# Kernel tuning notes

Hardware: AMD Instinct MI355X
Metric: run time of the kernel (lower is better)

The kernel has to match this reference:

```python
import jax, jax.numpy as jnp
import numpy as np
from jax import lax

N, D, H, O = 16384, 512, 1024, 512
G, E, K = 3, 4, 2
ALPHA = 0.01


def setup_inputs() -> dict:
    key = jax.random.key(0)
    ks = jax.random.split(key, 16)

    def lin(k, out_d, in_d):
        s = 1.0 / np.sqrt(in_d)
        return jax.random.uniform(k, (out_d, in_d), jnp.float32, -s, s)

    x = jax.random.normal(ks[0], (N, D), jnp.float32)
    Wm = lin(ks[1], G, D)
    bm = jnp.zeros((G,), jnp.float32)
    # group routers stacked: [G, E, D]
    Wr = jax.random.uniform(ks[2], (G, E, D), jnp.float32, -1 / np.sqrt(D), 1 / np.sqrt(D))
    br = jnp.zeros((G, E), jnp.float32)
    # expert params stacked over (group, expert)
    W1 = jax.random.uniform(ks[3], (G, E, H, D), jnp.float32, -1 / np.sqrt(D), 1 / np.sqrt(D))
    b1 = jnp.zeros((G, E, H), jnp.float32)
    W2 = jax.random.uniform(ks[4], (G, E, H, H), jnp.float32, -1 / np.sqrt(H), 1 / np.sqrt(H))
    b2 = jnp.zeros((G, E, H), jnp.float32)
    Wp = jax.random.uniform(ks[5], (G, E, H, D), jnp.float32, -1 / np.sqrt(D), 1 / np.sqrt(D))
    bp = jnp.zeros((G, E, H), jnp.float32)
    W3 = jax.random.uniform(ks[6], (G, E, O, H), jnp.float32, -1 / np.sqrt(H), 1 / np.sqrt(H))
    b3 = jnp.zeros((G, E, O), jnp.float32)
    return {"x": x, "Wm": Wm, "bm": bm, "Wr": Wr, "br": br,
            "W1": W1, "b1": b1, "W2": W2, "b2": b2,
            "Wp": Wp, "bp": bp, "W3": W3, "b3": b3}


def _expert(x, W1, b1, W2, b2, Wp, bp, W3, b3):
    # residual MLP (dropout in eval mode => identity)
    h = jax.nn.relu(x @ W1.T + b1)
    h = h @ W2.T + b2
    ident = x @ Wp.T + bp  # projection (input_dim != hidden_dim)
    h = jax.nn.relu(h + ident)
    return h @ W3.T + b3


def reference(x, Wm, bm, Wr, br, W1, b1, W2, b2, Wp, bp, W3, b3):
    n = x.shape[0]
    # ---- meta (top-1 group) routing ----
    meta_logits = x @ Wm.T + bm                         # [N, G]
    g = jnp.argmax(meta_logits, axis=1)                 # top-1 group per token
    pm = jax.nn.softmax(meta_logits, axis=1).mean(0)    # [G]
    aux = ALPHA * G * jnp.sum(pm * pm)
    # ---- per-group router logits, gathered for each token's group ----
    logits_all = jnp.einsum('nd,ged->nge', x, Wr) + br  # [N, G, E]
    sel = jnp.take_along_axis(logits_all, g[:, None, None], axis=1)[:, 0, :]  # [N, E]
    # ---- group-level load-balancing aux loss (over tokens in each group) ----
    probs = jax.nn.softmax(sel, axis=-1)                # [N, E]
    onehot_g = (g[:, None] == jnp.arange(G)[None, :])   # [N, G] bool
    cnt = onehot_g.sum(0)                               # [G]
    mean_g = (onehot_g.astype(x.dtype).T @ probs) / jnp.maximum(cnt, 1)[:, None].astype(x.dtype)
    aux = aux + jnp.sum(jnp.where(cnt > 0, ALPHA * E * jnp.sum(mean_g * mean_g, -1), 0.0))
    # ---- top-k expert weights within selected group (softmax over the k logits) ----
    vals, idx = lax.top_k(sel, K)                       # [N, K]
    w = jax.nn.softmax(vals, axis=-1)                   # [N, K]
    cw = jnp.zeros((n, E), x.dtype).at[jnp.arange(n)[:, None], idx].set(w)   # [N, E]
    combine = cw[:, None, :] * onehot_g[:, :, None].astype(x.dtype)          # [N, G, E]
    # ---- expert compute + combine (loop over the fixed small set of experts) ----
    out = jnp.zeros((n, O), x.dtype)
    for gi in range(G):
        for e in range(E):
            y = _expert(x, W1[gi, e], b1[gi, e], W2[gi, e], b2[gi, e],
                        Wp[gi, e], bp[gi, e], W3[gi, e], b3[gi, e])
            out = out + combine[:, gi, e:e + 1] * y
    return out, aux
```

## Files before the change

kernel.cpp:

```cpp
#include <hip/hip_runtime.h>
#include <hip/hip_bf16.h>

#define N_TOK 16384
#define DDIM  512
#define HDIM  1024
#define ODIM  512
#define NG    3
#define NE    4
#define NGE   12

typedef __bf16 bf16x8 __attribute__((ext_vector_type(8)));
typedef float  f32x4  __attribute__((ext_vector_type(4)));
typedef unsigned int u32;

__device__ __forceinline__ void gld_lds16(const void* gsrc, void* ldst) {
    __builtin_amdgcn_global_load_lds(
        (const __attribute__((address_space(1))) u32*)gsrc,
        (__attribute__((address_space(3))) u32*)ldst, 16, 0, 0);
}

static constexpr size_t OFF_WSLOT = 512;
static constexpr size_t OFF_ELIST = OFF_WSLOT + (size_t)N_TOK*2*4;
static constexpr size_t OFF_XBF   = 1048576;
static constexpr size_t OFF_W1    = OFF_XBF + (size_t)N_TOK*DDIM*2;
static constexpr size_t OFF_W2    = OFF_W1  + (size_t)NGE*HDIM*DDIM*2;
static constexpr size_t OFF_WP    = OFF_W2  + (size_t)NGE*HDIM*HDIM*2;
static constexpr size_t OFF_W3    = OFF_WP  + (size_t)NGE*HDIM*DDIM*2;
static constexpr size_t OFF_H1    = OFF_W3  + (size_t)NGE*ODIM*HDIM*2;
static constexpr size_t OFF_U     = OFF_H1  + (size_t)N_TOK*2*HDIM*2;
static constexpr size_t OFF_Y     = OFF_U   + (size_t)N_TOK*2*HDIM*2;
static constexpr size_t WS_NEED   = OFF_Y   + (size_t)N_TOK*2*ODIM*2;

__global__ void cast_all_k(const float* __restrict__ x,  const float* __restrict__ w1,
                           const float* __restrict__ w2, const float* __restrict__ wp,
                           const float* __restrict__ w3,
                           __bf16* xbf, __bf16* w1b, __bf16* w2b, __bf16* wpb, __bf16* w3b) {
    int tid = blockIdx.x * blockDim.x + threadIdx.x;
    int stride = gridDim.x * blockDim.x;
    auto seg = [&](const float* __restrict__ s, __bf16* __restrict__ d, int n4) {
        const float4* s4 = (const float4*)s;
        uint2* d4 = (uint2*)d;
        for (int i = tid; i < n4; i += stride) {
            float4 v = s4[i];
            union { __bf16 h[4]; uint2 u; } o;
            o.h[0] = (__bf16)v.x; o.h[1] = (__bf16)v.y;
            o.h[2] = (__bf16)v.z; o.h[3] = (__bf16)v.w;
            d4[i] = o.u;
        }
    };
    seg(x,  xbf, N_TOK*DDIM/4);
    seg(w1, w1b, NGE*HDIM*DDIM/4);
    seg(w2, w2b, NGE*HDIM*HDIM/4);
    seg(wp, wpb, NGE*HDIM*DDIM/4);
    seg(w3, w3b, NGE*ODIM*HDIM/4);
}

__global__ __launch_bounds__(256) void routing_k(
        const float* __restrict__ x,  const float* __restrict__ Wm,
        const float* __restrict__ bm, const float* __restrict__ Wr,
        const float* __restrict__ br,
        float* pmsum, float* psum, int* cnt, int* ecount,
        int* elist, float* wslot) {
    __shared__ float lpm[NG];
    __shared__ float lpsum[NGE];
    __shared__ int   lcnt[NG];
    __shared__ int   lec[NGE];
    __shared__ int   lbase[NGE];
    __shared__ int   lentry[NGE][64];

    int tid = threadIdx.x;
    if (tid < NG)  { lpm[tid] = 0.f; lcnt[tid] = 0; }
    if (tid < NGE) { lpsum[tid] = 0.f; lec[tid] = 0; }
    __syncthreads();

    int wid = tid >> 6, lane = tid & 63;

    #pragma unroll 1
    for (int i = 0; i < 16; ++i) {
        int t = blockIdx.x * 64 + i * 4 + wid;

        const float4* xr = (const float4*)(x + (size_t)t * DDIM);
        float4 xa = xr[lane*2], xb = xr[lane*2+1];

        float meta[NG];
        #pragma unroll
        for (int gi = 0; gi < NG; ++gi) {
            const float4* w = (const float4*)(Wm + gi*DDIM);
            float4 wa = w[lane*2], wb = w[lane*2+1];
            float s = xa.x*wa.x + xa.y*wa.y + xa.z*wa.z + xa.w*wa.w
                    + xb.x*wb.x + xb.y*wb.y + xb.z*wb.z + xb.w*wb.w;
            #pragma unroll
            for (int off = 32; off > 0; off >>= 1) s += __shfl_xor(s, off);
            meta[gi] = s + bm[gi];
        }
        int g = 0;
        if (meta[1] > meta[g]) g = 1;
        if (meta[2] > meta[g]) g = 2;

        float mm = fmaxf(meta[0], fmaxf(meta[1], meta[2]));
        float e0 = expf(meta[0]-mm), e1 = expf(meta[1]-mm), e2 = expf(meta[2]-mm);
        float inv = 1.f / (e0 + e1 + e2);

        float sel[NE];
        #pragma unroll
        for (int e = 0; e < NE; ++e) {
            const float4* w = (const float4*)(Wr + (size_t)(g*NE + e)*DDIM);
            float4 wa = w[lane*2], wb = w[lane*2+1];
            float s = xa.x*wa.x + xa.y*wa.y + xa.z*wa.z + xa.w*wa.w
                    + xb.x*wb.x + xb.y*wb.y + xb.z*wb.z + xb.w*wb.w;
            #pragma unroll
            for (int off = 32; off > 0; off >>= 1) s += __shfl_xor(s, off);
            sel[e] = s + br[g*NE + e];
        }
        float ms = fmaxf(fmaxf(sel[0],sel[1]), fmaxf(sel[2],sel[3]));
        float pe[NE]; float ss = 0.f;
        #pragma unroll
        for (int e = 0; e < NE; ++e) { pe[e] = expf(sel[e]-ms); ss += pe[e]; }
        float invs = 1.f / ss;

        int i0 = 0;
        #pragma unroll
        for (int e = 1; e < NE; ++e) if (sel[e] > sel[i0]) i0 = e;
        int i1 = (i0 == 0) ? 1 : 0;
        #pragma unroll
        for (int e = 0; e < NE; ++e) if (e != i0 && sel[e] > sel[i1]) i1 = e;
        float ew = expf(sel[i1] - sel[i0]);
        float wden = 1.f / (1.f + ew);

        if (lane == 0) {
            atomicAdd(&lpm[0], e0*inv);
            atomicAdd(&lpm[1], e1*inv);
            atomicAdd(&lpm[2], e2*inv);
            #pragma unroll
            for (int e = 0; e < NE; ++e) atomicAdd(&lpsum[g*NE + e], pe[e]*invs);
            atomicAdd(&lcnt[g], 1);
            int ee0 = g*NE + i0, ee1 = g*NE + i1;
            int p0 = atomicAdd(&lec[ee0], 1);
            lentry[ee0][p0] = t*2;
            int p1 = atomicAdd(&lec[ee1], 1);
            lentry[ee1][p1] = t*2 + 1;
            wslot[t*2]   = wden;
            wslot[t*2+1] = ew * wden;
        }
    }
    __syncthreads();

    if (tid < NG)  { atomicAdd(pmsum + tid, lpm[tid]); atomicAdd(cnt + tid, lcnt[tid]); }
    if (tid < NGE) { atomicAdd(psum + tid, lpsum[tid]);
                     lbase[tid] = atomicAdd(ecount + tid, lec[tid]); }
    __syncthreads();

    for (int e = wid; e < NGE; e += 4) {
        int c = lec[e], base = lbase[e];
        for (int j = lane; j < c; j += 64)
            elist[e*N_TOK + base + j] = lentry[e][j];
    }
}

__global__ void finalize_aux_k(const float* pmsum, const float* psum, const int* cnt,
                               float* outAux) {
    if (threadIdx.x != 0 || blockIdx.x != 0) return;
    float s = 0.f;
    for (int i = 0; i < NG; ++i) { float p = pmsum[i] / (float)N_TOK; s += p*p; }
    float aux = 0.01f * NG * s;
    for (int gg = 0; gg < NG; ++gg) {
        int c = cnt[gg];
        if (c > 0) {
            float s2 = 0.f;
            for (int e = 0; e < NE; ++e) { float m = psum[gg*NE+e] / (float)c; s2 += m*m; }
            aux += 0.01f * NE * s2;
        }
    }
    *outAux = aux;
}

template<int NDIM, bool RELU, bool TWOPASS>
__global__ __launch_bounds__(256) void expert_gemm_k(
        const __bf16* __restrict__ A1, int shift1, int k1, const __bf16* __restrict__ B1,
        const __bf16* __restrict__ A2, int shift2, int k2, const __bf16* __restrict__ B2,
        const float* __restrict__ bias1, const float* __restrict__ bias2,
        __bf16* __restrict__ Out,
        const int* __restrict__ ecount, const int* __restrict__ elist) {
    int ge = blockIdx.z;
    int cntE = ecount[ge];
    int m0 = blockIdx.x * 128;
    if (m0 >= cntE) return;
    int n0 = blockIdx.y * 128;

    __shared__ __align__(16) char ldsA[16384];
    __shared__ __align__(16) char ldsB[16384];
    __shared__ int ents[128];

    int tid = threadIdx.x;
    if (tid < 128) {
        int r = m0 + tid;
        if (r >= cntE) r = cntE - 1;
        ents[tid] = elist[ge*N_TOK + r];
    }
    __syncthreads();

    int lane = tid & 63, wv = tid >> 6;
    int wm = wv >> 1, wn = wv & 1;
    int lr = lane & 15, lg = lane >> 4;
    int rl = lane >> 3;
    int csw = (lane & 7) ^ rl;
    int rsw = lr & 7;

    f32x4 acc[4][4] = {};

    #pragma unroll
    for (int pass = 0; pass < (TWOPASS ? 2 : 1); ++pass) {
        const __bf16* A  = pass ? A2 : A1;
        const __bf16* Bm = pass ? B2 : B1;
        int kdim  = pass ? k2 : k1;
        int shift = pass ? shift2 : shift1;
        size_t rowB = (size_t)kdim * 2;
        const char* Bbase = (const char*)(Bm + (size_t)ge * NDIM * kdim) + (size_t)n0 * rowB;

        const char* sA[4]; const char* sB[4];
        #pragma unroll
        for (int j = 0; j < 4; ++j) {
            int r = (wv*4 + j)*8 + rl;
            sA[j] = (const char*)A + (size_t)(ents[r] >> shift) * rowB + (size_t)csw*16;
            sB[j] = Bbase + (size_t)r * rowB + (size_t)csw*16;
        }

        for (int kt = 0; kt < kdim; kt += 64) {
            size_t ko = (size_t)kt * 2;
            #pragma unroll
            for (int j = 0; j < 4; ++j) {
                gld_lds16(sA[j] + ko, ldsA + (wv*4 + j)*1024);
                gld_lds16(sB[j] + ko, ldsB + (wv*4 + j)*1024);
            }
            __syncthreads();
            #pragma unroll
            for (int kk = 0; kk < 2; ++kk) {
                bf16x8 av[4], bv[4];
                #pragma unroll
                for (int mi = 0; mi < 4; ++mi) {
                    int ar = wm*64 + mi*16 + lr;
                    av[mi] = *(const bf16x8*)(ldsA + ar*128 + ((((kk*4+lg) ^ rsw)) << 4));
                }
                #pragma unroll
                for (int ni = 0; ni < 4; ++ni) {
                    int br_ = wn*64 + ni*16 + lr;
                    bv[ni] = *(const bf16x8*)(ldsB + br_*128 + ((((kk*4+lg) ^ rsw)) << 4));
                }
                #pragma unroll
                for (int mi = 0; mi < 4; ++mi)
                    #pragma unroll
                    for (int ni = 0; ni < 4; ++ni)
                        acc[mi][ni] = __builtin_amdgcn_mfma_f32_16x16x32_bf16(
                            av[mi], bv[ni], acc[mi][ni], 0, 0, 0);
            }
            __syncthreads();
        }
    }

    #pragma unroll
    for (int ni = 0; ni < 4; ++ni) {
        int col = n0 + wn*64 + ni*16 + lr;
        float b = bias1[(size_t)ge*NDIM + col];
        if constexpr (TWOPASS) b += bias2[(size_t)ge*NDIM + col];
        #pragma unroll
        for (int mi = 0; mi < 4; ++mi) {
            #pragma unroll
            for (int j = 0; j < 4; ++j) {
                int rloc = wm*64 + mi*16 + lg*4 + j;
                if (m0 + rloc < cntE) {
                    float v = acc[mi][ni][j] + b;
                    if constexpr (RELU) v = fmaxf(v, 0.f);
                    Out[(size_t)ents[rloc] * NDIM + col] = (__bf16)v;
                }
            }
        }
    }
}

__global__ void combine_k(const __bf16* __restrict__ Y, const float* __restrict__ wslot,
                          float* __restrict__ out) {
    int idx = blockIdx.x * blockDim.x + threadIdx.x;
    int t = idx >> 6;
    int o = (idx & 63) * 8;
    bf16x8 y0 = *(const bf16x8*)(Y + (size_t)(2*t)   * ODIM + o);
    bf16x8 y1 = *(const bf16x8*)(Y + (size_t)(2*t+1) * ODIM + o);
    float w0 = wslot[2*t], w1 = wslot[2*t+1];
    float4 r0, r1;
    r0.x = w0*(float)y0[0] + w1*(float)y1[0];
    r0.y = w0*(float)y0[1] + w1*(float)y1[1];
    r0.z = w0*(float)y0[2] + w1*(float)y1[2];
    r0.w = w0*(float)y0[3] + w1*(float)y1[3];
    r1.x = w0*(float)y0[4] + w1*(float)y1[4];
    r1.y = w0*(float)y0[5] + w1*(float)y1[5];
    r1.z = w0*(float)y0[6] + w1*(float)y1[6];
    r1.w = w0*(float)y0[7] + w1*(float)y1[7];
    float* op = out + (size_t)t * ODIM + o;
    ((float4*)op)[0] = r0;
    ((float4*)op)[1] = r1;
}

extern "C" void kernel_launch(void* const* d_in, const int* in_sizes, int n_in,
                              void* d_out, int out_size, void* d_ws, size_t ws_size,
                              hipStream_t stream) {
    const float* x  = (const float*)d_in[0];
    const float* Wm = (const float*)d_in[1];
    const float* bm = (const float*)d_in[2];
    const float* Wr = (const float*)d_in[3];
    const float* br = (const float*)d_in[4];
    const float* W1 = (const float*)d_in[5];
    const float* b1 = (const float*)d_in[6];
    const float* W2 = (const float*)d_in[7];
    const float* b2 = (const float*)d_in[8];
    const float* Wp = (const float*)d_in[9];
    const float* bp = (const float*)d_in[10];
    const float* W3 = (const float*)d_in[11];
    const float* b3 = (const float*)d_in[12];

    if (ws_size < WS_NEED) return;

    char* ws = (char*)d_ws;
    float* outp = (float*)d_out;

    float* pmsum  = (float*)ws;
    float* psum   = (float*)ws + 4;
    int*   cnt    = (int*)ws + 16;
    int*   ecount = (int*)ws + 20;
    float* wslot  = (float*)(ws + OFF_WSLOT);
    int*   elist  = (int*)(ws + OFF_ELIST);
    __bf16* xbf = (__bf16*)(ws + OFF_XBF);
    __bf16* w1b = (__bf16*)(ws + OFF_W1);
    __bf16* w2b = (__bf16*)(ws + OFF_W2);
    __bf16* wpb = (__bf16*)(ws + OFF_WP);
    __bf16* w3b = (__bf16*)(ws + OFF_W3);
    __bf16* H1  = (__bf16*)(ws + OFF_H1);
    __bf16* U   = (__bf16*)(ws + OFF_U);
    __bf16* Y   = (__bf16*)(ws + OFF_Y);

    hipMemsetAsync(d_ws, 0, 512, stream);

    cast_all_k<<<4096, 256, 0, stream>>>(x, W1, W2, Wp, W3, xbf, w1b, w2b, wpb, w3b);

    routing_k<<<256, 256, 0, stream>>>(x, Wm, bm, Wr, br,
                                       pmsum, psum, cnt, ecount, elist, wslot);

    finalize_aux_k<<<1, 64, 0, stream>>>(pmsum, psum, cnt, outp + (size_t)N_TOK*ODIM);

    dim3 gA(128, HDIM/128, NGE);
    expert_gemm_k<HDIM, true, false><<<gA, 256, 0, stream>>>(
        xbf, 1, DDIM, w1b, nullptr, 0, 0, nullptr, b1, nullptr, H1, ecount, elist);

    expert_gemm_k<HDIM, true, true><<<gA, 256, 0, stream>>>(
        H1, 0, HDIM, w2b, xbf, 1, DDIM, wpb, b2, bp, U, ecount, elist);

    dim3 gC(128, ODIM/128, NGE);
    expert_gemm_k<ODIM, false, false><<<gC, 256, 0, stream>>>(
        U, 0, HDIM, w3b, nullptr, 0, 0, nullptr, b3, nullptr, Y, ecount, elist);

    combine_k<<<4096, 256, 0, stream>>>(Y, wslot, outp);
}
```

Baseline: 486.2 us.

## Compact expert GEMM grid via task list and double-buffer LDS K-loop

finalize_aux_k now writes a compact list of (expert, row-tile) tasks, so the GEMM grids launch a fixed task-capacity dimension instead of 128×12 blocks, most of which exit immediately. The GEMM K loop gains double-buffered LDS: the next K tile is loaded asynchronously while MFMAs run on the current one, with one barrier per step. The two passes of the fused W2/Wp GEMM are merged into one pipelined stream. This doubles LDS use to about 64KB per block, which may cut occupancy, and the task list is built serially by a single thread.

```diff
diff --git a/kernel.cpp b/kernel.cpp
--- a/kernel.cpp
+++ b/kernel.cpp
@@ -8,6 +8,7 @@
 #define NG    3
 #define NE    4
 #define NGE   12
+#define TASK_CAP 272
 
 typedef __bf16 bf16x8 __attribute__((ext_vector_type(8)));
 typedef float  f32x4  __attribute__((ext_vector_type(4)));
@@ -21,6 +22,7 @@
 
 static constexpr size_t OFF_WSLOT = 512;
 static constexpr size_t OFF_ELIST = OFF_WSLOT + (size_t)N_TOK*2*4;
+static constexpr size_t OFF_TASK  = 917504;
 static constexpr size_t OFF_XBF   = 1048576;
 static constexpr size_t OFF_W1    = OFF_XBF + (size_t)N_TOK*DDIM*2;
 static constexpr size_t OFF_W2    = OFF_W1  + (size_t)NGE*HDIM*DDIM*2;
@@ -158,6 +160,7 @@
 }
 
 __global__ void finalize_aux_k(const float* pmsum, const float* psum, const int* cnt,
+                               const int* ecount, int2* tasks, int* ntasks,
                                float* outAux) {
     if (threadIdx.x != 0 || blockIdx.x != 0) return;
     float s = 0.f;
@@ -172,6 +175,12 @@
         }
     }
     *outAux = aux;
+    int nt = 0;
+    for (int ge = 0; ge < NGE; ++ge) {
+        int c = ecount[ge];
+        for (int m0 = 0; m0 < c; m0 += 128) tasks[nt++] = make_int2(ge, m0);
+    }
+    *ntasks = nt;
 }
 
 template<int NDIM, bool RELU, bool TWOPASS>
@@ -180,15 +189,16 @@
         const __bf16* __restrict__ A2, int shift2, int k2, const __bf16* __restrict__ B2,
         const float* __restrict__ bias1, const float* __restrict__ bias2,
         __bf16* __restrict__ Out,
-        const int* __restrict__ ecount, const int* __restrict__ elist) {
-    int ge = blockIdx.z;
+        const int* __restrict__ ecount, const int* __restrict__ elist,
+        const int2* __restrict__ tasks, const int* __restrict__ ntasks) {
+    if (blockIdx.x >= *ntasks) return;
+    int2 tk = tasks[blockIdx.x];
+    int ge = tk.x, m0 = tk.y;
     int cntE = ecount[ge];
-    int m0 = blockIdx.x * 128;
-    if (m0 >= cntE) return;
     int n0 = blockIdx.y * 128;
 
-    __shared__ __align__(16) char ldsA[16384];
-    __shared__ __align__(16) char ldsB[16384];
+    __shared__ __align__(16) char ldsA[2][16384];
+    __shared__ __align__(16) char ldsB[2][16384];
     __shared__ int ents[128];
 
     int tid = threadIdx.x;
@@ -206,55 +216,80 @@
     int csw = (lane & 7) ^ rl;
     int rsw = lr & 7;
 
+    const char* sA1[4]; const char* sB1[4];
+    const char* sA2[4]; const char* sB2[4];
+    size_t rowB1 = (size_t)k1 * 2;
+    const char* Bb1 = (const char*)(B1 + (size_t)ge * NDIM * k1) + (size_t)n0 * rowB1;
+    #pragma unroll
+    for (int j = 0; j < 4; ++j) {
+        int r = wv*32 + j*8 + rl;
+        sA1[j] = (const char*)A1 + (size_t)(ents[r] >> shift1) * rowB1 + (size_t)csw*16;
+        sB1[j] = Bb1 + (size_t)r * rowB1 + (size_t)csw*16;
+    }
+    if constexpr (TWOPASS) {
+        size_t rowB2 = (size_t)k2 * 2;
+        const char* Bb2 = (const char*)(B2 + (size_t)ge * NDIM * k2) + (size_t)n0 * rowB2;
+        #pragma unroll
+        for (int j = 0; j < 4; ++j) {
+            int r = wv*32 + j*8 + rl;
+            sA2[j] = (const char*)A2 + (size_t)(ents[r] >> shift2) * rowB2 + (size_t)csw*16;
+            sB2[j] = Bb2 + (size_t)r * rowB2 + (size_t)csw*16;
+        }
+    }
+
+    int nk1 = k1 >> 6;
+    int nk  = TWOPASS ? nk1 + (k2 >> 6) : nk1;
+
+    auto stage = [&](int s) {
+        int b = s & 1;
+        if (!TWOPASS || s < nk1) {
+            size_t ko = (size_t)s << 7;
+            #pragma unroll
+            for (int j = 0; j < 4; ++j) {
+                gld_lds16(sA1[j] + ko, ldsA[b] + (wv*4 + j)*1024);
+                gld_lds16(sB1[j] + ko, ldsB[b] + (wv*4 + j)*1024);
+            }
+        } else {
+            size_t ko = (size_t)(s - nk1) << 7;
+            #pragma unroll
+            for (int j = 0; j < 4; ++j) {
+                gld_lds16(sA2[j] + ko, ldsA[b] + (wv*4 + j)*1024);
+                gld_lds16(sB2[j] + ko, ldsB[b] + (wv*4 + j)*1024);
+            }
+        }
+    };
+
     f32x4 acc[4][4] = {};
 
-    #pragma unroll
-    for (int pass = 0; pass < (TWOPASS ? 2 : 1); ++pass) {
-        const __bf16* A  = pass ? A2 : A1;
-        const __bf16* Bm = pass ? B2 : B1;
-        int kdim  = pass ? k2 : k1;
-        int shift = pass ? shift2 : shift1;
-        size_t rowB = (size_t)kdim * 2;
-        const char* Bbase = (const char*)(Bm + (size_t)ge * NDIM * kdim) + (size_t)n0 * rowB;
-
-        const char* sA[4]; const char* sB[4];
-        #pragma unroll
-        for (int j = 0; j < 4; ++j) {
-            int r = (wv*4 + j)*8 + rl;
-            sA[j] = (const char*)A + (size_t)(ents[r] >> shift) * rowB + (size_t)csw*16;
-            sB[j] = Bbase + (size_t)r * rowB + (size_t)csw*16;
-        }
-
-        for (int kt = 0; kt < kdim; kt += 64) {
-            size_t ko = (size_t)kt * 2;
-            #pragma unroll
-            for (int j = 0; j < 4; ++j) {
-                gld_lds16(sA[j] + ko, ldsA + (wv*4 + j)*1024);
-                gld_lds16(sB[j] + ko, ldsB + (wv*4 + j)*1024);
+    stage(0);
+    __syncthreads();
+
+    #pragma unroll 1
+    for (int s = 0; s < nk; ++s) {
+        if (s + 1 < nk) stage(s + 1);
+        const char* bA = ldsA[s & 1];
+        const char* bB = ldsB[s & 1];
+        #pragma unroll
+        for (int kk = 0; kk < 2; ++kk) {
+            bf16x8 av[4], bv[4];
+            #pragma unroll
+            for (int mi = 0; mi < 4; ++mi) {
+                int ar = wm*64 + mi*16 + lr;
+                av[mi] = *(const bf16x8*)(bA + ar*128 + ((((kk*4+lg) ^ rsw)) << 4));
             }
-            __syncthreads();
-            #pragma unroll
-            for (int kk = 0; kk < 2; ++kk) {
-                bf16x8 av[4], bv[4];
+            #pragma unroll
+            for (int ni = 0; ni < 4; ++ni) {
+                int br_ = wn*64 + ni*16 + lr;
+                bv[ni] = *(const bf16x8*)(bB + br_*128 + ((((kk*4+lg) ^ rsw)) << 4));
+            }
+            #pragma unroll
+            for (int mi = 0; mi < 4; ++mi)
                 #pragma unroll
-                for (int mi = 0; mi < 4; ++mi) {
-                    int ar = wm*64 + mi*16 + lr;
-                    av[mi] = *(const bf16x8*)(ldsA + ar*128 + ((((kk*4+lg) ^ rsw)) << 4));
-                }
-                #pragma unroll
-                for (int ni = 0; ni < 4; ++ni) {
-                    int br_ = wn*64 + ni*16 + lr;
-                    bv[ni] = *(const bf16x8*)(ldsB + br_*128 + ((((kk*4+lg) ^ rsw)) << 4));
-                }
-                #pragma unroll
-                for (int mi = 0; mi < 4; ++mi)
-                    #pragma unroll
-                    for (int ni = 0; ni < 4; ++ni)
-                        acc[mi][ni] = __builtin_amdgcn_mfma_f32_16x16x32_bf16(
-                            av[mi], bv[ni], acc[mi][ni], 0, 0, 0);
-            }
-            __syncthreads();
-        }
+                for (int ni = 0; ni < 4; ++ni)
+                    acc[mi][ni] = __builtin_amdgcn_mfma_f32_16x16x32_bf16(
+                        av[mi], bv[ni], acc[mi][ni], 0, 0, 0);
+        }
+        __syncthreads();
     }
 
     #pragma unroll
@@ -325,8 +360,10 @@
     float* psum   = (float*)ws + 4;
     int*   cnt    = (int*)ws + 16;
     int*   ecount = (int*)ws + 20;
+    int*   ntasks = (int*)ws + 34;
     float* wslot  = (float*)(ws + OFF_WSLOT);
     int*   elist  = (int*)(ws + OFF_ELIST);
+    int2*  tasks  = (int2*)(ws + OFF_TASK);
     __bf16* xbf = (__bf16*)(ws + OFF_XBF);
     __bf16* w1b = (__bf16*)(ws + OFF_W1);
     __bf16* w2b = (__bf16*)(ws + OFF_W2);
@@ -343,18 +380,22 @@
     routing_k<<<256, 256, 0, stream>>>(x, Wm, bm, Wr, br,
                                        pmsum, psum, cnt, ecount, elist, wslot);
 
-    finalize_aux_k<<<1, 64, 0, stream>>>(pmsum, psum, cnt, outp + (size_t)N_TOK*ODIM);
-
-    dim3 gA(128, HDIM/128, NGE);
+    finalize_aux_k<<<1, 64, 0, stream>>>(pmsum, psum, cnt, ecount, tasks, ntasks,
+                                         outp + (size_t)N_TOK*ODIM);
+
+    dim3 gA(TASK_CAP, HDIM/128, 1);
     expert_gemm_k<HDIM, true, false><<<gA, 256, 0, stream>>>(
-        xbf, 1, DDIM, w1b, nullptr, 0, 0, nullptr, b1, nullptr, H1, ecount, elist);
+        xbf, 1, DDIM, w1b, nullptr, 0, 0, nullptr, b1, nullptr, H1,
+        ecount, elist, tasks, ntasks);
 
     expert_gemm_k<HDIM, true, true><<<gA, 256, 0, stream>>>(
-        H1, 0, HDIM, w2b, xbf, 1, DDIM, wpb, b2, bp, U, ecount, elist);
-
-    dim3 gC(128, ODIM/128, NGE);
+        H1, 0, HDIM, w2b, xbf, 1, DDIM, wpb, b2, bp, U,
+        ecount, elist, tasks, ntasks);
+
+    dim3 gC(TASK_CAP, ODIM/128, 1);
     expert_gemm_k<ODIM, false, false><<<gC, 256, 0, stream>>>(
-        U, 0, HDIM, w3b, nullptr, 0, 0, nullptr, b3, nullptr, Y, ecount, elist);
+        U, 0, HDIM, w3b, nullptr, 0, 0, nullptr, b3, nullptr, Y,
+        ecount, elist, tasks, ntasks);
 
     combine_k<<<4096, 256, 0, stream>>>(Y, wslot, outp);
 }
```

Result: faster. 474.3 us (-2.5%).
